# Kernel tuning notes

Hardware: AMD Instinct MI355X
Metric: run time of the kernel (lower is better)

## Reference

```python
import jax, jax.numpy as jnp
import numpy as np

MAX_IT = 10
LAMBDA_ROF = 4.0
SIGMA = 1.0 / (7.0 * 0.01)
TAU = 0.01
THETA = 0.5
M, N = 2048, 2048


def forward_grad(x):
    """x: [1,M,N] -> [2,M,N]; forward differences, zero at last col/row."""
    gh = jnp.pad(x[0, :, 1:] - x[0, :, :-1], ((0, 0), (0, 1)))  # horizontal
    gv = jnp.pad(x[0, 1:, :] - x[0, :-1, :], ((0, 1), (0, 0)))  # vertical
    return jnp.stack([gh, gv], axis=0)


def backward_div(y):
    """y: [2,M,N] -> [1,M,N]; adjoint backward-difference divergence."""
    yh, yv = y[0], y[1]
    d_h = jnp.concatenate([yh[:, :1], yh[:, 1:-1] - yh[:, :-2], -yh[:, -2:-1]], axis=1)
    d_v = jnp.concatenate([yv[:1, :], yv[1:-1, :] - yv[:-2, :], -yv[-2:-1, :]], axis=0)
    return (d_h + d_v)[None]  # [1,M,N]


def prox_linf_ball(p, r):
    # Torch original builds m1/m2 from p.data (no grad flow) -> stop_gradient.
    m1 = jnp.maximum(p - r, 0.0)
    m2 = jnp.maximum(-p - r, 0.0)
    return p - jax.lax.stop_gradient(m1 - m2)  # == clamp(p, -r, r) in value


def setup_inputs() -> dict:
    key = jax.random.key(0)
    k1, k2 = jax.random.split(key)
    img_obs = jax.random.uniform(k1, (1, M, N), dtype=jnp.float32)
    w1 = jnp.array([0.5], dtype=jnp.float32)  # nn.Parameter [1]
    w2 = jnp.array([0.4], dtype=jnp.float32)  # nn.Parameter [1]
    return {"img_obs": img_obs, "w1": w1, "w2": w2}


def reference(img_obs, w1, w2):
    x = img_obs
    x_tilde = img_obs
    y = forward_grad(x)  # [2,M,N]
    # w_term built from y.data in torch -> constant wrt autodiff
    w_term = jax.lax.stop_gradient(jnp.exp(-jnp.abs(y)))
    w = w1[0] + w2[0] * w_term  # [2,M,N]
    for _ in range(MAX_IT):
        # dual weighted update + L-inf prox
        y = y + SIGMA * w * forward_grad(x_tilde)
        y = prox_linf_ball(y, 1.0)
        # primal weighted update (ROF)
        x_old = x
        x = (x + TAU * backward_div(w * y) + LAMBDA_ROF * TAU * img_obs) / (1.0 + LAMBDA_ROF * TAU)
        # primal over-relaxation
        x_tilde = x + THETA * (x - x_old)
    return x_tilde
```

## Files before the change

kernel.cpp:

```cpp
#include <hip/hip_runtime.h>


namespace {
constexpr int M = 2048, N = 2048;
constexpr float SIGMA     = 1.0f / (7.0f * 0.01f);
constexpr float TAUIS     = 0.01f * (7.0f * 0.01f);
constexpr float LT        = 4.0f * 0.01f;
constexpr float INV_DEN   = 1.0f / (1.0f + 4.0f * 0.01f);
constexpr float TAUIS_ID  = TAUIS * INV_DEN;
constexpr float LT_ID     = LT * INV_DEN;
constexpr int TW = 64, TH = 64;
constexpr int PC = 88;
constexpr int PR = 84;
constexpr int UPR = 22;
constexpr int PROC = 83;
constexpr int NU = PROC * UPR;
constexpr int NT = 1024;
constexpr int NPASS = 2;
constexpr int GY = M / TH;
}

typedef _Float16 h4 __attribute__((ext_vector_type(4)));
typedef float    f2 __attribute__((ext_vector_type(2)));
typedef unsigned uint32;

__device__ inline h4 h4splat(float v) {
    _Float16 s = (_Float16)v;
    return (h4){s, s, s, s};
}
__device__ inline int imax(int a, int b) { return a > b ? a : b; }
__device__ inline uint32 abit(uint32 hi, uint32 lo) {
    return __builtin_amdgcn_alignbit(hi, lo, 16);
}
__device__ inline h4 clamp1(h4 v) {
    return __builtin_elementwise_min(
               __builtin_elementwise_max(v, h4splat(-1.f)), h4splat(1.f));
}

__global__ __launch_bounds__(NT, 8) void pd_fused(
    const float* __restrict__ img, float* __restrict__ out,
    const float* __restrict__ w1p, const float* __restrict__ w2p)
{
    __shared__ __align__(16) _Float16 sXT16[PR * PC];
    __shared__ __align__(16) _Float16 sQV[PR * PC];
    __shared__ __align__(16) _Float16 sCI[PR * PC];
    __shared__ __align__(16) _Float16 sSWH[PR * PC];
    __shared__ __align__(16) _Float16 sSWV[PR * PC];
    __shared__ __align__(16) _Float16 sQH3[1840];

    const int tid  = threadIdx.x;
    const int c0 = blockIdx.x * TW, r0 = blockIdx.y * TH;
    const int gr0 = r0 - 10, gc0 = c0 - 12;
    const float w1 = w1p[0], w2 = w2p[0];

    int dth_[NPASS];
    #pragma unroll
    for (int p = 0; p < NPASS; ++p) {
        int u = tid + p * NT;
        int li = u / UPR, lc = (u - li * UPR) * 4;
        int d = imax(imax(9 - li, li - (TH + 9)), imax(8 - lc, lc - 75));
        d = imax(d, 0);
        if (u >= NU) d = 100;
        dth_[p] = d;
    }

    #pragma unroll
    for (int p = 0; p < NPASS; ++p) {
        int su = tid + p * NT;
        if (su < PR * UPR) {
            int li = su / UPR, uj = su - li * UPR;
            int gi = gr0 + li, gj = gc0 + uj * 4;
            float4 v = make_float4(0.f, 0.f, 0.f, 0.f);
            if ((unsigned)gi < (unsigned)M && (unsigned)gj <= (unsigned)(N - 4))
                v = *(const float4*)&img[(size_t)gi * N + gj];
            h4 h; h[0] = (_Float16)v.x; h[1] = (_Float16)v.y;
                  h[2] = (_Float16)v.z; h[3] = (_Float16)v.w;
            *(h4*)&sXT16[su * 4] = h;
        }
    }
    __syncthreads();

    f2 xr2[NPASS][2];
    h4 xt16[NPASS], yh[NPASS], yv[NPASS], qH[NPASS];

    #pragma unroll
    for (int p = 0; p < NPASS; ++p) {
        int u = tid + p * NT;
        if (u < NU) {
            int bF = u * 4;
            int li = u / UPR;
            int gi = gr0 + li, gjb = gc0 + (u - li * UPR) * 4;
            h4 c16 = *(const h4*)&sXT16[bF];
            uint32 rrp = *(const uint32*)&sXT16[bF + 4];
            h4 dn = *(const h4*)&sXT16[bF + PC];
            uint2 xu = __builtin_bit_cast(uint2, c16);
            h4 xsh = __builtin_bit_cast(h4,
                         make_uint2(abit(xu.y, xu.x), abit(rrp, xu.y)));
            bool rok = (unsigned)gi < (unsigned)M;
            bool vok = rok && (gi < M - 1);
            h4 qv, swhv, swvv, civ;
            #pragma unroll
            for (int l = 0; l < 4; ++l) {
                int gj = gjb + l;
                bool cok = (unsigned)gj < (unsigned)N;
                bool hok = rok && cok && (gj < N - 1);
                bool vk  = vok && cok;
                float xf  = (float)c16[l];
                float ghf = hok ? (float)xsh[l] - xf : 0.f;
                float gvf = vk  ? (float)dn[l]  - xf : 0.f;
                float wh = fmaf(w2, __expf(-fabsf(ghf)), w1);
                float wv = fmaf(w2, __expf(-fabsf(gvf)), w1);
                float y0h = fminf(fmaxf(ghf * fmaf(SIGMA, wh, 1.f), -1.f), 1.f);
                float y0v = fminf(fmaxf(gvf * fmaf(SIGMA, wv, 1.f), -1.f), 1.f);
                float sh = hok ? SIGMA * wh : 0.f;
                float sv = vk  ? SIGMA * wv : 0.f;
                yh[p][l]   = (_Float16)y0h;  yv[p][l] = (_Float16)y0v;
                swhv[l]    = (_Float16)sh;   swvv[l]  = (_Float16)sv;
                qH[p][l]   = (_Float16)(sh * y0h);
                qv[l]      = (_Float16)(sv * y0v);
                civ[l]     = (_Float16)(LT_ID * xf);
                xr2[p][l >> 1][l & 1] = xf;
            }
            xt16[p] = c16;
            *(h4*)&sSWH[bF] = swhv;
            *(h4*)&sSWV[bF] = swvv;
            *(h4*)&sCI[bF]  = civ;
            *(h4*)&sQV[bF]  = qv;
            sQH3[u] = qH[p][3];
        }
    }
    __syncthreads();

    auto dual = [&](int rem) {
        #pragma unroll
        for (int p = 0; p < NPASS; ++p) {
            if (rem >= dth_[p]) {
                int bF = (tid + p * NT) * 4;
                uint32 rrp = *(const uint32*)&sXT16[bF + 4];
                h4 dn  = *(const h4*)&sXT16[bF + PC];
                h4 swh = *(const h4*)&sSWH[bF];
                h4 swv = *(const h4*)&sSWV[bF];
                uint2 xu = __builtin_bit_cast(uint2, xt16[p]);
                h4 xsh = __builtin_bit_cast(h4,
                             make_uint2(abit(xu.y, xu.x), abit(rrp, xu.y)));
                h4 ghh = xsh - xt16[p];
                h4 gvh = dn  - xt16[p];
                h4 nh = clamp1(yh[p] + swh * ghh);
                h4 nv = clamp1(yv[p] + swv * gvh);
                yh[p] = nh; yv[p] = nv;
                h4 qh = swh * nh;
                h4 qv = swv * nv;
                qH[p] = qh;
                *(h4*)&sQV[bF] = qv;
                sQH3[bF >> 2] = qh[3];
            }
        }
    };

    const f2 kID  = {INV_DEN,  INV_DEN};
    const f2 kTS  = {TAUIS_ID, TAUIS_ID};
    const f2 k15  = {1.5f, 1.5f};
    const f2 km05 = {-0.5f, -0.5f};
    auto primal = [&](int rem, bool last) {
        #pragma unroll
        for (int p = 0; p < NPASS; ++p) {
            if (rem >= dth_[p]) {
                int u = tid + p * NT, bF = u * 4;
                int bu = (bF >= UPR * 4) ? bF - PC : bF;
                h4 qvu = *(const h4*)&sQV[bu];
                h4 qv  = *(const h4*)&sQV[bF];
                h4 civ = *(const h4*)&sCI[bF];
                uint32 qhl = *(const unsigned short*)&sQH3[imax(u - 1, 0)];
                uint2 qu = __builtin_bit_cast(uint2, qH[p]);
                h4 qsh = __builtin_bit_cast(h4,
                             make_uint2(abit(qu.x, qhl << 16), abit(qu.y, qu.x)));
                h4 dvg = (qH[p] - qsh) + (qv - qvu);
                f2 dv0 = {(float)dvg[0], (float)dvg[1]};
                f2 dv1 = {(float)dvg[2], (float)dvg[3]};
                f2 ci0 = {(float)civ[0], (float)civ[1]};
                f2 ci1 = {(float)civ[2], (float)civ[3]};
                f2 xo0 = xr2[p][0], xo1 = xr2[p][1];
                f2 xn0 = __builtin_elementwise_fma(kID, xo0,
                             __builtin_elementwise_fma(kTS, dv0, ci0));
                f2 xn1 = __builtin_elementwise_fma(kID, xo1,
                             __builtin_elementwise_fma(kTS, dv1, ci1));
                xr2[p][0] = xn0; xr2[p][1] = xn1;
                f2 xt0 = __builtin_elementwise_fma(k15, xn0, xo0 * km05);
                f2 xt1 = __builtin_elementwise_fma(k15, xn1, xo1 * km05);
                if (!last) {
                    h4 nx; nx[0] = (_Float16)xt0[0]; nx[1] = (_Float16)xt0[1];
                           nx[2] = (_Float16)xt1[0]; nx[3] = (_Float16)xt1[1];
                    xt16[p] = nx;
                    *(h4*)&sXT16[bF] = nx;
                } else {
                    int li = u / UPR, uj = u - li * UPR;
                    int gi = gr0 + li;
                    if (li >= 10 && uj >= 3 && uj <= 18 && gi < M) {
                        *(float4*)&out[(size_t)gi * N + (gc0 + uj * 4)] =
                            make_float4(xt0[0], xt0[1], xt1[0], xt1[1]);
                    }
                }
            }
        }
    };

    primal(9, false);
    __syncthreads();
    #pragma unroll 1
    for (int t = 1; t < 10; ++t) {
        int rem = 9 - t;
        dual(rem);
        __syncthreads();
        primal(rem, t == 9);
        __syncthreads();
    }
}

extern "C" void kernel_launch(void* const* d_in, const int* in_sizes, int n_in,
                              void* d_out, int out_size, void* d_ws, size_t ws_size,
                              hipStream_t stream)
{
    const float* img = (const float*)d_in[0];
    const float* w1  = (const float*)d_in[1];
    const float* w2  = (const float*)d_in[2];
    float* out = (float*)d_out;

    dim3 grid(N / TW, GY);
    pd_fused<<<grid, NT, 0, stream>>>(img, out, w1, w2);
}
```

Baseline: 107.9 us.

## Keep per-pixel weights and constants in registers, use 768 threads with three passes

```diff
diff --git a/kernel.cpp b/kernel.cpp
--- a/kernel.cpp
+++ b/kernel.cpp
@@ -15,8 +15,8 @@
 constexpr int UPR = 22;
 constexpr int PROC = 83;
 constexpr int NU = PROC * UPR;
-constexpr int NT = 1024;
-constexpr int NPASS = 2;
+constexpr int NT = 768;
+constexpr int NPASS = 3;
 constexpr int GY = M / TH;
 }
 
@@ -37,21 +37,24 @@
                __builtin_elementwise_max(v, h4splat(-1.f)), h4splat(1.f));
 }
 
-__global__ __launch_bounds__(NT, 8) void pd_fused(
+__global__ __launch_bounds__(NT, 6) void pd_fused(
     const float* __restrict__ img, float* __restrict__ out,
     const float* __restrict__ w1p, const float* __restrict__ w2p)
 {
     __shared__ __align__(16) _Float16 sXT16[PR * PC];
     __shared__ __align__(16) _Float16 sQV[PR * PC];
-    __shared__ __align__(16) _Float16 sCI[PR * PC];
-    __shared__ __align__(16) _Float16 sSWH[PR * PC];
-    __shared__ __align__(16) _Float16 sSWV[PR * PC];
-    __shared__ __align__(16) _Float16 sQH3[1840];
+    __shared__ __align__(16) _Float16 sQH3[1832];
 
     const int tid  = threadIdx.x;
     const int c0 = blockIdx.x * TW, r0 = blockIdx.y * TH;
     const int gr0 = r0 - 10, gc0 = c0 - 12;
     const float w1 = w1p[0], w2 = w2p[0];
+
+    char* bXT8 = (char*)sXT16 + tid * 8;
+    char* bQV8 = (char*)sQV   + tid * 8;
+    char* bQ3  = (char*)sQH3  + tid * 2;
+    const char* bQVu0 = (char*)sQV + (tid >= UPR ? tid - UPR : tid) * 8;
+    const int   q3o0  = imax(tid - 1, 0);
 
     int dth_[NPASS];
     #pragma unroll
@@ -75,30 +78,31 @@
                 v = *(const float4*)&img[(size_t)gi * N + gj];
             h4 h; h[0] = (_Float16)v.x; h[1] = (_Float16)v.y;
                   h[2] = (_Float16)v.z; h[3] = (_Float16)v.w;
-            *(h4*)&sXT16[su * 4] = h;
+            *(h4*)(bXT8 + p * 6144) = h;
         }
     }
     __syncthreads();
 
-    f2 xr2[NPASS][2];
-    h4 xt16[NPASS], yh[NPASS], yv[NPASS], qH[NPASS];
+    f2 xr2[NPASS][2], ci2[NPASS][2];
+    h4 xt16[NPASS], yh[NPASS], yv[NPASS], qH[NPASS],
+       swh[NPASS], swv[NPASS], qvr[NPASS];
 
     #pragma unroll
     for (int p = 0; p < NPASS; ++p) {
         int u = tid + p * NT;
         if (u < NU) {
-            int bF = u * 4;
             int li = u / UPR;
             int gi = gr0 + li, gjb = gc0 + (u - li * UPR) * 4;
-            h4 c16 = *(const h4*)&sXT16[bF];
-            uint32 rrp = *(const uint32*)&sXT16[bF + 4];
-            h4 dn = *(const h4*)&sXT16[bF + PC];
+            const char* bx = bXT8 + p * 6144;
+            h4 c16 = *(const h4*)bx;
+            uint2 rr = *(const uint2*)(bx + 8);
+            h4 dn = *(const h4*)(bx + 176);
             uint2 xu = __builtin_bit_cast(uint2, c16);
             h4 xsh = __builtin_bit_cast(h4,
-                         make_uint2(abit(xu.y, xu.x), abit(rrp, xu.y)));
+                         make_uint2(abit(xu.y, xu.x), abit(rr.x, xu.y)));
             bool rok = (unsigned)gi < (unsigned)M;
             bool vok = rok && (gi < M - 1);
-            h4 qv, swhv, swvv, civ;
+            h4 qv;
             #pragma unroll
             for (int l = 0; l < 4; ++l) {
                 int gj = gjb + l;
@@ -114,19 +118,17 @@
                 float y0v = fminf(fmaxf(gvf * fmaf(SIGMA, wv, 1.f), -1.f), 1.f);
                 float sh = hok ? SIGMA * wh : 0.f;
                 float sv = vk  ? SIGMA * wv : 0.f;
-                yh[p][l]   = (_Float16)y0h;  yv[p][l] = (_Float16)y0v;
-                swhv[l]    = (_Float16)sh;   swvv[l]  = (_Float16)sv;
-                qH[p][l]   = (_Float16)(sh * y0h);
-                qv[l]      = (_Float16)(sv * y0v);
-                civ[l]     = (_Float16)(LT_ID * xf);
+                yh[p][l]  = (_Float16)y0h;  yv[p][l] = (_Float16)y0v;
+                swh[p][l] = (_Float16)sh;   swv[p][l] = (_Float16)sv;
+                qH[p][l]  = (_Float16)(sh * y0h);
+                qv[l]     = (_Float16)(sv * y0v);
+                ci2[p][l >> 1][l & 1] = LT_ID * xf;
                 xr2[p][l >> 1][l & 1] = xf;
             }
             xt16[p] = c16;
-            *(h4*)&sSWH[bF] = swhv;
-            *(h4*)&sSWV[bF] = swvv;
-            *(h4*)&sCI[bF]  = civ;
-            *(h4*)&sQV[bF]  = qv;
-            sQH3[u] = qH[p][3];
+            qvr[p]  = qv;
+            *(h4*)(bQV8 + p * 6144) = qv;
+            *(_Float16*)(bQ3 + p * 1536) = qH[p][3];
         }
     }
     __syncthreads();
@@ -135,24 +137,22 @@
         #pragma unroll
         for (int p = 0; p < NPASS; ++p) {
             if (rem >= dth_[p]) {
-                int bF = (tid + p * NT) * 4;
-                uint32 rrp = *(const uint32*)&sXT16[bF + 4];
-                h4 dn  = *(const h4*)&sXT16[bF + PC];
-                h4 swh = *(const h4*)&sSWH[bF];
-                h4 swv = *(const h4*)&sSWV[bF];
+                const char* bx = bXT8 + p * 6144;
+                uint2 rr = *(const uint2*)(bx + 8);
+                h4 dn = *(const h4*)(bx + 176);
                 uint2 xu = __builtin_bit_cast(uint2, xt16[p]);
                 h4 xsh = __builtin_bit_cast(h4,
-                             make_uint2(abit(xu.y, xu.x), abit(rrp, xu.y)));
+                             make_uint2(abit(xu.y, xu.x), abit(rr.x, xu.y)));
                 h4 ghh = xsh - xt16[p];
                 h4 gvh = dn  - xt16[p];
-                h4 nh = clamp1(yh[p] + swh * ghh);
-                h4 nv = clamp1(yv[p] + swv * gvh);
+                h4 nh = clamp1(yh[p] + swh[p] * ghh);
+                h4 nv = clamp1(yv[p] + swv[p] * gvh);
                 yh[p] = nh; yv[p] = nv;
-                h4 qh = swh * nh;
-                h4 qv = swv * nv;
-                qH[p] = qh;
-                *(h4*)&sQV[bF] = qv;
-                sQH3[bF >> 2] = qh[3];
+                h4 qh = swh[p] * nh;
+                h4 qv = swv[p] * nv;
+                qH[p] = qh; qvr[p] = qv;
+                *(h4*)(bQV8 + p * 6144) = qv;
+                *(_Float16*)(bQ3 + p * 1536) = qh[3];
             }
         }
     };
@@ -165,25 +165,22 @@
         #pragma unroll
         for (int p = 0; p < NPASS; ++p) {
             if (rem >= dth_[p]) {
-                int u = tid + p * NT, bF = u * 4;
-                int bu = (bF >= UPR * 4) ? bF - PC : bF;
-                h4 qvu = *(const h4*)&sQV[bu];
-                h4 qv  = *(const h4*)&sQV[bF];
-                h4 civ = *(const h4*)&sCI[bF];
-                uint32 qhl = *(const unsigned short*)&sQH3[imax(u - 1, 0)];
+                h4 qvu = (p == 0) ? *(const h4*)bQVu0
+                                  : *(const h4*)(bQV8 + p * 6144 - 176);
+                uint32 qhl = (p == 0)
+                    ? *(const unsigned short*)&sQH3[q3o0]
+                    : *(const unsigned short*)(bQ3 + p * 1536 - 2);
                 uint2 qu = __builtin_bit_cast(uint2, qH[p]);
                 h4 qsh = __builtin_bit_cast(h4,
                              make_uint2(abit(qu.x, qhl << 16), abit(qu.y, qu.x)));
-                h4 dvg = (qH[p] - qsh) + (qv - qvu);
+                h4 dvg = (qH[p] - qsh) + (qvr[p] - qvu);
                 f2 dv0 = {(float)dvg[0], (float)dvg[1]};
                 f2 dv1 = {(float)dvg[2], (float)dvg[3]};
-                f2 ci0 = {(float)civ[0], (float)civ[1]};
-                f2 ci1 = {(float)civ[2], (float)civ[3]};
                 f2 xo0 = xr2[p][0], xo1 = xr2[p][1];
                 f2 xn0 = __builtin_elementwise_fma(kID, xo0,
-                             __builtin_elementwise_fma(kTS, dv0, ci0));
+                             __builtin_elementwise_fma(kTS, dv0, ci2[p][0]));
                 f2 xn1 = __builtin_elementwise_fma(kID, xo1,
-                             __builtin_elementwise_fma(kTS, dv1, ci1));
+                             __builtin_elementwise_fma(kTS, dv1, ci2[p][1]));
                 xr2[p][0] = xn0; xr2[p][1] = xn1;
                 f2 xt0 = __builtin_elementwise_fma(k15, xn0, xo0 * km05);
                 f2 xt1 = __builtin_elementwise_fma(k15, xn1, xo1 * km05);
@@ -191,8 +188,9 @@
                     h4 nx; nx[0] = (_Float16)xt0[0]; nx[1] = (_Float16)xt0[1];
                            nx[2] = (_Float16)xt1[0]; nx[3] = (_Float16)xt1[1];
                     xt16[p] = nx;
-                    *(h4*)&sXT16[bF] = nx;
+                    *(h4*)(bXT8 + p * 6144) = nx;
                 } else {
+                    int u = tid + p * NT;
                     int li = u / UPR, uj = u - li * UPR;
                     int gi = gr0 + li;
                     if (li >= 10 && uj >= 3 && uj <= 18 && gi < M) {
```

After: 123.6 us. 14.5% more time.

## Process 8 halves per thread in a single pass with unified LDS layout

Applied to the files above, without the earlier changes.

```diff
diff --git a/kernel.cpp b/kernel.cpp
--- a/kernel.cpp
+++ b/kernel.cpp
@@ -12,148 +12,149 @@
 constexpr int TW = 64, TH = 64;
 constexpr int PC = 88;
 constexpr int PR = 84;
-constexpr int UPR = 22;
+constexpr int UPR = 11;
 constexpr int PROC = 83;
 constexpr int NU = PROC * UPR;
+constexpr int NS = PR * UPR;
 constexpr int NT = 1024;
-constexpr int NPASS = 2;
 constexpr int GY = M / TH;
-}
-
-typedef _Float16 h4 __attribute__((ext_vector_type(4)));
+constexpr int OQ7 = 0;
+constexpr int OXT = 1856;
+constexpr int OQV = OXT + 14784;
+constexpr int OCI = OQV + 14784;
+constexpr int OSH = OCI + 14784;
+constexpr int OSV = OSH + 14784;
+constexpr int LDSZ = OSV + 14784;
+}
+
+typedef _Float16 h8 __attribute__((ext_vector_type(8)));
 typedef float    f2 __attribute__((ext_vector_type(2)));
 typedef unsigned uint32;
 
-__device__ inline h4 h4splat(float v) {
+__device__ inline h8 h8splat(float v) {
     _Float16 s = (_Float16)v;
-    return (h4){s, s, s, s};
+    return (h8){s, s, s, s, s, s, s, s};
 }
 __device__ inline int imax(int a, int b) { return a > b ? a : b; }
 __device__ inline uint32 abit(uint32 hi, uint32 lo) {
     return __builtin_amdgcn_alignbit(hi, lo, 16);
 }
-__device__ inline h4 clamp1(h4 v) {
+__device__ inline h8 clamp1(h8 v) {
     return __builtin_elementwise_min(
-               __builtin_elementwise_max(v, h4splat(-1.f)), h4splat(1.f));
+               __builtin_elementwise_max(v, h8splat(-1.f)), h8splat(1.f));
 }
 
 __global__ __launch_bounds__(NT, 8) void pd_fused(
     const float* __restrict__ img, float* __restrict__ out,
     const float* __restrict__ w1p, const float* __restrict__ w2p)
 {
-    __shared__ __align__(16) _Float16 sXT16[PR * PC];
-    __shared__ __align__(16) _Float16 sQV[PR * PC];
-    __shared__ __align__(16) _Float16 sCI[PR * PC];
-    __shared__ __align__(16) _Float16 sSWH[PR * PC];
-    __shared__ __align__(16) _Float16 sSWV[PR * PC];
-    __shared__ __align__(16) _Float16 sQH3[1840];
-
-    const int tid  = threadIdx.x;
+    __shared__ __align__(16) char sB[LDSZ];
+
+    const int tid = threadIdx.x;
     const int c0 = blockIdx.x * TW, r0 = blockIdx.y * TH;
     const int gr0 = r0 - 10, gc0 = c0 - 12;
     const float w1 = w1p[0], w2 = w2p[0];
 
-    int dth_[NPASS];
-    #pragma unroll
-    for (int p = 0; p < NPASS; ++p) {
-        int u = tid + p * NT;
-        int li = u / UPR, lc = (u - li * UPR) * 4;
-        int d = imax(imax(9 - li, li - (TH + 9)), imax(8 - lc, lc - 75));
+    char* b16 = sB + tid * 16;
+    char* bQ7 = sB + OQ7 + tid * 2;
+    const char* bQVu = b16 + OQV - (tid >= UPR ? 176 : 0);
+    const char* bQ7l = sB + OQ7 + imax(tid - 1, 0) * 2;
+
+    int dth;
+    {
+        int li = tid / UPR, lc = (tid - li * UPR) * 8;
+        int d = imax(imax(9 - li, li - (TH + 9)), imax(4 - lc, lc - 75));
         d = imax(d, 0);
-        if (u >= NU) d = 100;
-        dth_[p] = d;
-    }
-
-    #pragma unroll
-    for (int p = 0; p < NPASS; ++p) {
-        int su = tid + p * NT;
-        if (su < PR * UPR) {
-            int li = su / UPR, uj = su - li * UPR;
-            int gi = gr0 + li, gj = gc0 + uj * 4;
-            float4 v = make_float4(0.f, 0.f, 0.f, 0.f);
-            if ((unsigned)gi < (unsigned)M && (unsigned)gj <= (unsigned)(N - 4))
-                v = *(const float4*)&img[(size_t)gi * N + gj];
-            h4 h; h[0] = (_Float16)v.x; h[1] = (_Float16)v.y;
-                  h[2] = (_Float16)v.z; h[3] = (_Float16)v.w;
-            *(h4*)&sXT16[su * 4] = h;
+        if (tid >= NU) d = 100;
+        dth = d;
+    }
+
+    if (tid < NS) {
+        int li = tid / UPR, uj = tid - li * UPR;
+        int gi = gr0 + li, gj0 = gc0 + uj * 8;
+        float4 v0 = make_float4(0.f, 0.f, 0.f, 0.f);
+        float4 v1 = make_float4(0.f, 0.f, 0.f, 0.f);
+        bool rok = (unsigned)gi < (unsigned)M;
+        if (rok && (unsigned)gj0 <= (unsigned)(N - 4))
+            v0 = *(const float4*)&img[(size_t)gi * N + gj0];
+        if (rok && (unsigned)(gj0 + 4) <= (unsigned)(N - 4))
+            v1 = *(const float4*)&img[(size_t)gi * N + gj0 + 4];
+        h8 h;
+        h[0] = (_Float16)v0.x; h[1] = (_Float16)v0.y;
+        h[2] = (_Float16)v0.z; h[3] = (_Float16)v0.w;
+        h[4] = (_Float16)v1.x; h[5] = (_Float16)v1.y;
+        h[6] = (_Float16)v1.z; h[7] = (_Float16)v1.w;
+        *(h8*)(b16 + OXT) = h;
+    }
+    __syncthreads();
+
+    f2 xr2[4];
+    h8 xt16, yh, yv, qH;
+
+    if (tid < NU) {
+        int li = tid / UPR;
+        int gi = gr0 + li, gjb = gc0 + (tid - li * UPR) * 8;
+        h8 c16 = *(const h8*)(b16 + OXT);
+        uint32 rr = *(const uint32*)(b16 + OXT + 16);
+        h8 dn = *(const h8*)(b16 + OXT + 176);
+        uint4 xu = __builtin_bit_cast(uint4, c16);
+        h8 xsh = __builtin_bit_cast(h8,
+                     make_uint4(abit(xu.y, xu.x), abit(xu.z, xu.y),
+                                abit(xu.w, xu.z), abit(rr, xu.w)));
+        bool rok = (unsigned)gi < (unsigned)M;
+        bool vok = rok && (gi < M - 1);
+        h8 qv, swh, swv, civ;
+        #pragma unroll
+        for (int l = 0; l < 8; ++l) {
+            int gj = gjb + l;
+            bool cok = (unsigned)gj < (unsigned)N;
+            bool hok = rok && cok && (gj < N - 1);
+            bool vk  = vok && cok;
+            float xf  = (float)c16[l];
+            float ghf = hok ? (float)xsh[l] - xf : 0.f;
+            float gvf = vk  ? (float)dn[l]  - xf : 0.f;
+            float wh = fmaf(w2, __expf(-fabsf(ghf)), w1);
+            float wv = fmaf(w2, __expf(-fabsf(gvf)), w1);
+            float y0h = fminf(fmaxf(ghf * fmaf(SIGMA, wh, 1.f), -1.f), 1.f);
+            float y0v = fminf(fmaxf(gvf * fmaf(SIGMA, wv, 1.f), -1.f), 1.f);
+            float sh = hok ? SIGMA * wh : 0.f;
+            float sv = vk  ? SIGMA * wv : 0.f;
+            yh[l]  = (_Float16)y0h;  yv[l] = (_Float16)y0v;
+            swh[l] = (_Float16)sh;   swv[l] = (_Float16)sv;
+            qH[l]  = (_Float16)(sh * y0h);
+            qv[l]  = (_Float16)(sv * y0v);
+            civ[l] = (_Float16)(LT_ID * xf);
+            xr2[l >> 1][l & 1] = xf;
         }
+        xt16 = c16;
+        *(h8*)(b16 + OSH) = swh;
+        *(h8*)(b16 + OSV) = swv;
+        *(h8*)(b16 + OCI) = civ;
+        *(h8*)(b16 + OQV) = qv;
+        *(_Float16*)bQ7 = qH[7];
     }
     __syncthreads();
 
-    f2 xr2[NPASS][2];
-    h4 xt16[NPASS], yh[NPASS], yv[NPASS], qH[NPASS];
-
-    #pragma unroll
-    for (int p = 0; p < NPASS; ++p) {
-        int u = tid + p * NT;
-        if (u < NU) {
-            int bF = u * 4;
-            int li = u / UPR;
-            int gi = gr0 + li, gjb = gc0 + (u - li * UPR) * 4;
-            h4 c16 = *(const h4*)&sXT16[bF];
-            uint32 rrp = *(const uint32*)&sXT16[bF + 4];
-            h4 dn = *(const h4*)&sXT16[bF + PC];
-            uint2 xu = __builtin_bit_cast(uint2, c16);
-            h4 xsh = __builtin_bit_cast(h4,
-                         make_uint2(abit(xu.y, xu.x), abit(rrp, xu.y)));
-            bool rok = (unsigned)gi < (unsigned)M;
-            bool vok = rok && (gi < M - 1);
-            h4 qv, swhv, swvv, civ;
-            #pragma unroll
-            for (int l = 0; l < 4; ++l) {
-                int gj = gjb + l;
-                bool cok = (unsigned)gj < (unsigned)N;
-                bool hok = rok && cok && (gj < N - 1);
-                bool vk  = vok && cok;
-                float xf  = (float)c16[l];
-                float ghf = hok ? (float)xsh[l] - xf : 0.f;
-                float gvf = vk  ? (float)dn[l]  - xf : 0.f;
-                float wh = fmaf(w2, __expf(-fabsf(ghf)), w1);
-                float wv = fmaf(w2, __expf(-fabsf(gvf)), w1);
-                float y0h = fminf(fmaxf(ghf * fmaf(SIGMA, wh, 1.f), -1.f), 1.f);
-                float y0v = fminf(fmaxf(gvf * fmaf(SIGMA, wv, 1.f), -1.f), 1.f);
-                float sh = hok ? SIGMA * wh : 0.f;
-                float sv = vk  ? SIGMA * wv : 0.f;
-                yh[p][l]   = (_Float16)y0h;  yv[p][l] = (_Float16)y0v;
-                swhv[l]    = (_Float16)sh;   swvv[l]  = (_Float16)sv;
-                qH[p][l]   = (_Float16)(sh * y0h);
-                qv[l]      = (_Float16)(sv * y0v);
-                civ[l]     = (_Float16)(LT_ID * xf);
-                xr2[p][l >> 1][l & 1] = xf;
-            }
-            xt16[p] = c16;
-            *(h4*)&sSWH[bF] = swhv;
-            *(h4*)&sSWV[bF] = swvv;
-            *(h4*)&sCI[bF]  = civ;
-            *(h4*)&sQV[bF]  = qv;
-            sQH3[u] = qH[p][3];
-        }
-    }
-    __syncthreads();
-
     auto dual = [&](int rem) {
-        #pragma unroll
-        for (int p = 0; p < NPASS; ++p) {
-            if (rem >= dth_[p]) {
-                int bF = (tid + p * NT) * 4;
-                uint32 rrp = *(const uint32*)&sXT16[bF + 4];
-                h4 dn  = *(const h4*)&sXT16[bF + PC];
-                h4 swh = *(const h4*)&sSWH[bF];
-                h4 swv = *(const h4*)&sSWV[bF];
-                uint2 xu = __builtin_bit_cast(uint2, xt16[p]);
-                h4 xsh = __builtin_bit_cast(h4,
-                             make_uint2(abit(xu.y, xu.x), abit(rrp, xu.y)));
-                h4 ghh = xsh - xt16[p];
-                h4 gvh = dn  - xt16[p];
-                h4 nh = clamp1(yh[p] + swh * ghh);
-                h4 nv = clamp1(yv[p] + swv * gvh);
-                yh[p] = nh; yv[p] = nv;
-                h4 qh = swh * nh;
-                h4 qv = swv * nv;
-                qH[p] = qh;
-                *(h4*)&sQV[bF] = qv;
-                sQH3[bF >> 2] = qh[3];
-            }
+        if (rem >= dth) {
+            uint32 rr = *(const uint32*)(b16 + OXT + 16);
+            h8 dn  = *(const h8*)(b16 + OXT + 176);
+            h8 swh = *(const h8*)(b16 + OSH);
+            h8 swv = *(const h8*)(b16 + OSV);
+            uint4 xu = __builtin_bit_cast(uint4, xt16);
+            h8 xsh = __builtin_bit_cast(h8,
+                         make_uint4(abit(xu.y, xu.x), abit(xu.z, xu.y),
+                                    abit(xu.w, xu.z), abit(rr, xu.w)));
+            h8 ghh = xsh - xt16;
+            h8 gvh = dn  - xt16;
+            h8 nh = clamp1(yh + swh * ghh);
+            h8 nv = clamp1(yv + swv * gvh);
+            yh = nh; yv = nv;
+            h8 qh = swh * nh;
+            h8 qv = swv * nv;
+            qH = qh;
+            *(h8*)(b16 + OQV) = qv;
+            *(_Float16*)bQ7 = qh[7];
         }
     };
 
@@ -162,43 +163,46 @@
     const f2 k15  = {1.5f, 1.5f};
     const f2 km05 = {-0.5f, -0.5f};
     auto primal = [&](int rem, bool last) {
-        #pragma unroll
-        for (int p = 0; p < NPASS; ++p) {
-            if (rem >= dth_[p]) {
-                int u = tid + p * NT, bF = u * 4;
-                int bu = (bF >= UPR * 4) ? bF - PC : bF;
-                h4 qvu = *(const h4*)&sQV[bu];
-                h4 qv  = *(const h4*)&sQV[bF];
-                h4 civ = *(const h4*)&sCI[bF];
-                uint32 qhl = *(const unsigned short*)&sQH3[imax(u - 1, 0)];
-                uint2 qu = __builtin_bit_cast(uint2, qH[p]);
-                h4 qsh = __builtin_bit_cast(h4,
-                             make_uint2(abit(qu.x, qhl << 16), abit(qu.y, qu.x)));
-                h4 dvg = (qH[p] - qsh) + (qv - qvu);
-                f2 dv0 = {(float)dvg[0], (float)dvg[1]};
-                f2 dv1 = {(float)dvg[2], (float)dvg[3]};
-                f2 ci0 = {(float)civ[0], (float)civ[1]};
-                f2 ci1 = {(float)civ[2], (float)civ[3]};
-                f2 xo0 = xr2[p][0], xo1 = xr2[p][1];
-                f2 xn0 = __builtin_elementwise_fma(kID, xo0,
-                             __builtin_elementwise_fma(kTS, dv0, ci0));
-                f2 xn1 = __builtin_elementwise_fma(kID, xo1,
-                             __builtin_elementwise_fma(kTS, dv1, ci1));
-                xr2[p][0] = xn0; xr2[p][1] = xn1;
-                f2 xt0 = __builtin_elementwise_fma(k15, xn0, xo0 * km05);
-                f2 xt1 = __builtin_elementwise_fma(k15, xn1, xo1 * km05);
-                if (!last) {
-                    h4 nx; nx[0] = (_Float16)xt0[0]; nx[1] = (_Float16)xt0[1];
-                           nx[2] = (_Float16)xt1[0]; nx[3] = (_Float16)xt1[1];
-                    xt16[p] = nx;
-                    *(h4*)&sXT16[bF] = nx;
-                } else {
-                    int li = u / UPR, uj = u - li * UPR;
-                    int gi = gr0 + li;
-                    if (li >= 10 && uj >= 3 && uj <= 18 && gi < M) {
-                        *(float4*)&out[(size_t)gi * N + (gc0 + uj * 4)] =
-                            make_float4(xt0[0], xt0[1], xt1[0], xt1[1]);
-                    }
+        if (rem >= dth) {
+            h8 qvu = *(const h8*)bQVu;
+            h8 qvo = *(const h8*)(b16 + OQV);
+            h8 civ = *(const h8*)(b16 + OCI);
+            uint32 qhl = *(const unsigned short*)bQ7l;
+            uint4 qu = __builtin_bit_cast(uint4, qH);
+            h8 qsh = __builtin_bit_cast(h8,
+                         make_uint4(abit(qu.x, qhl << 16), abit(qu.y, qu.x),
+                                    abit(qu.z, qu.y),      abit(qu.w, qu.z)));
+            h8 dvg = (qH - qsh) + (qvo - qvu);
+            f2 xtv[4];
+            #pragma unroll
+            for (int i = 0; i < 4; ++i) {
+                f2 dv = {(float)dvg[2 * i], (float)dvg[2 * i + 1]};
+                f2 ci = {(float)civ[2 * i], (float)civ[2 * i + 1]};
+                f2 xo = xr2[i];
+                f2 xn = __builtin_elementwise_fma(kID, xo,
+                            __builtin_elementwise_fma(kTS, dv, ci));
+                xr2[i] = xn;
+                xtv[i] = __builtin_elementwise_fma(k15, xn, xo * km05);
+            }
+            if (!last) {
+                h8 nx;
+                #pragma unroll
+                for (int i = 0; i < 4; ++i) {
+                    nx[2 * i]     = (_Float16)xtv[i][0];
+                    nx[2 * i + 1] = (_Float16)xtv[i][1];
+                }
+                xt16 = nx;
+                *(h8*)(b16 + OXT) = nx;
+            } else {
+                int li = tid / UPR, uj = tid - li * UPR;
+                int gi = gr0 + li, gj0 = gc0 + uj * 8;
+                if (li >= 10) {
+                    if (uj >= 2)
+                        *(float4*)&out[(size_t)gi * N + gj0] =
+                            make_float4(xtv[0][0], xtv[0][1], xtv[1][0], xtv[1][1]);
+                    if (uj <= 8)
+                        *(float4*)&out[(size_t)gi * N + gj0 + 4] =
+                            make_float4(xtv[2][0], xtv[2][1], xtv[3][0], xtv[3][1]);
                 }
             }
         }
```

New measurement: 113.0 us. 1.05x slower.
